# Kernel optimization log

Hardware: AMD Instinct MI355X
Metric: run time of the kernel (lower is better)

The kernel has to match this reference:

```python
import jax, jax.numpy as jnp
import numpy as np

MAX_ITER = 3


def setup_inputs() -> dict:
    key = jax.random.key(0)
    B, S = 8, 128
    k1, k2, k3, k4 = jax.random.split(key, 4)
    return {
        's_edge': jax.random.normal(k1, (B, S, S), jnp.float32),
        's_sib': jax.random.normal(k2, (B, S, S, S), jnp.float32),
        's_cop': jax.random.normal(k3, (B, S, S, S), jnp.float32),
        's_grd': jax.random.normal(k4, (B, S, S, S), jnp.float32),
        'mask': jnp.ones((B, S, S), dtype=bool),
    }


def _msg_update(q, m_old, s):
    # q: [2,S,S,B]; m_old, s: [2|_,S,S,S,B]
    m = q[:, :, :, None, :] - m_old                      # [2,S,S,S,B]
    low = jnp.logaddexp(m[0], m[1])                      # label-0 message
    high = jnp.logaddexp(m[0], m[1] + s)                 # label-1 message (adds 2nd-order score)
    z = jnp.logaddexp(low, high)                         # log_softmax over the 2-way label axis
    return jnp.stack([low - z, high - z])


def _lbp(s_edge, s_sib, s_cop, s_grd, mask, max_iter):
    B, S, _ = mask.shape
    hs = jnp.broadcast_to(jnp.arange(S)[:, None], (S, S))   # row index i
    ms = jnp.broadcast_to(jnp.arange(S)[None, :], (S, S))   # col index j
    maskT = jnp.transpose(mask, (2, 1, 0))                   # [S,S,B] (j,i,B)
    mask2o = maskT[:, None] & maskT[:, :, None]              # [S,S,S,B]
    ar = jnp.arange(S)
    mask2o = mask2o & (hs[..., None] != ar)[..., None]
    mask2o = mask2o & (ms[..., None] != ar)[..., None]
    mask2o = mask2o.astype(s_edge.dtype)                     # [S,S,S,B]

    # s_edge -> [2, j, i, B]; second-order scores -> [j, i, k, B]
    se = jnp.stack([jnp.zeros_like(s_edge), s_edge])
    se = jnp.transpose(se, (0, 3, 2, 1))
    sib = jnp.transpose(s_sib, (2, 1, 3, 0))
    cop = jnp.transpose(s_cop, (2, 1, 3, 0))
    grd = jnp.transpose(s_grd, (2, 1, 3, 0))

    q = se
    zero = jnp.zeros((2, S, S, S, B), dtype=s_edge.dtype)
    m_sib, m_cop, m_grd = zero, zero, zero
    for _ in range(max_iter):
        q = jax.nn.log_softmax(q, axis=0)
        m_sib = _msg_update(q, m_sib, sib)
        m_cop = _msg_update(q, m_cop, cop)
        m_grd = _msg_update(q, m_grd, grd)
        agg = jnp.swapaxes(m_sib + m_cop + m_grd, 2, 3) * mask2o
        q = se + agg.sum(3)                                  # [2,S,S,B]
    return jnp.transpose(q, (3, 2, 1, 0))                     # [B,S,S,2]


def reference(s_edge, s_sib, s_cop, s_grd, mask):
    logits = _lbp(s_edge, s_sib, s_cop, s_grd, mask, MAX_ITER)
    return jax.nn.softmax(logits, axis=-1)[..., 1]            # marginals [B,S,S]
```

## Files before the change

kernel.cpp:

```cpp
#include <hip/hip_runtime.h>


#define TS 128
#define SS (TS * TS)
#define NREG 3

typedef float    f2v __attribute__((ext_vector_type(2)));
typedef _Float16 h2v __attribute__((ext_vector_type(2)));

constexpr float LOG2E = 1.4426950408889634f;

__device__ __forceinline__ float rcpf(float x)   { return __builtin_amdgcn_rcpf(x); }
__device__ __forceinline__ float clampe(float e) { return fminf(fmaxf(e, -126.0f), 60.0f); }
__device__ __forceinline__ float rfl(float x) {
    return __int_as_float(__builtin_amdgcn_readfirstlane(__float_as_int(x)));
}

__global__ void mask_probe(const unsigned char* __restrict__ m, int n, int* __restrict__ f) {
    __shared__ int s1, s23;
    if (threadIdx.x == 0) { s1 = 0; s23 = 0; }
    __syncthreads();
    unsigned a1 = 0, a23 = 0;
    const int n16 = n >> 4;
    const uint4* m4 = (const uint4*)m;
    for (int i = threadIdx.x; i < n16; i += 1024) {
        const uint4 v = m4[i];
        const unsigned o = v.x | v.y | v.z | v.w;
        a1  |= o & 0x0000FF00u;
        a23 |= o & 0xFFFF0000u;
    }
    for (int i = (n16 << 4) + threadIdx.x; i < n; i += 1024) {
        const unsigned char b = m[i];
        const int r = i & 3;
        if (r == 1) a1 |= b;
        if (r >= 2) a23 |= b;
    }
    if (__any(a1 != 0)  && (threadIdx.x & 63) == 0) atomicOr(&s1, 1);
    if (__any(a23 != 0) && (threadIdx.x & 63) == 0) atomicOr(&s23, 1);
    __syncthreads();
    if (threadIdx.x == 0) { f[0] = s1; f[1] = s23; }
}

__global__ __launch_bounds__(1024, 8)
__attribute__((amdgpu_waves_per_eu(8, 8)))
void lbp_fused(const float* __restrict__ s_edge,
               const float* __restrict__ sib,
               const float* __restrict__ cop,
               const float* __restrict__ grd,
               const void* __restrict__ mask,
               const int* __restrict__ flags,
               float* __restrict__ outp)
{
    __shared__ _Float16 FLs[8 - NREG][16][TS];
    __shared__ _Float16 FLc[8 - NREG][16][TS];
    __shared__ _Float16 FLg[8 - NREG][16][TS];
    __shared__ float red[16][TS];
    __shared__ float q0s[TS], p1s[TS], r1s[TS], g1s[TS], g2s[TS];
    __shared__ unsigned char mrow[TS];

    const int bj = blockIdx.x;
    const int b  = bj >> 7;
    const int j  = bj & (TS - 1);
    const int t  = threadIdx.x;
    const int lane = t & 63;
    const int wv = t >> 6;
    const int ka = 2 * lane, kb = 2 * lane + 1;

    if (t < TS) {
        const int i = t;
        const int idx = (b * TS + i) * TS + j;
        const float q0 = LOG2E * s_edge[idx];
        q0s[i] = q0;
        const int f1 = flags[0], f23 = flags[1];
        unsigned char mv;
        if (f1)       mv = ((const unsigned char*)mask)[idx] != 0;
        else if (f23) mv = ((const float*)mask)[idx] != 0.0f;
        else          mv = ((const int*)mask)[idx]   != 0;
        mrow[i] = mv;
        const float p1 = exp2f(clampe(-q0));
        p1s[i] = p1;
        r1s[i] = rcpf(1.0f + p1);
    }
    __syncthreads();

    const size_t gbase = (size_t)b * (TS * SS) + (size_t)j * TS + (size_t)wv * SS + ka;

    h2v Fs[NREG], Fc[NREG], Fg[NREG];
    float a0 = 0.0f, a1 = 0.0f;
    f2v vs = *(const f2v*)(sib + gbase);
    f2v vc = *(const f2v*)(cop + gbase);
    f2v vg = *(const f2v*)(grd + gbase);
    #pragma unroll
    for (int r = 0; r < 8; ++r) {
        f2v nvs, nvc, nvg;
        if (r < 7) {
            const size_t g = gbase + (size_t)(16 * (r + 1)) * SS;
            nvs = *(const f2v*)(sib + g);
            nvc = *(const f2v*)(cop + g);
            nvg = *(const f2v*)(grd + g);
        }
        const int i = 16 * r + wv;
        f2v fs, fc, fg;
        fs[0] = exp2f(LOG2E * vs[0]);  fs[1] = exp2f(LOG2E * vs[1]);
        fc[0] = exp2f(LOG2E * vc[0]);  fc[1] = exp2f(LOG2E * vc[1]);
        fg[0] = exp2f(LOG2E * vg[0]);  fg[1] = exp2f(LOG2E * vg[1]);
        if (r < NREG) {
            Fs[r] = __builtin_convertvector(fs, h2v);
            Fc[r] = __builtin_convertvector(fc, h2v);
            Fg[r] = __builtin_convertvector(fg, h2v);
        } else {
            *(h2v*)&FLs[r - NREG][wv][ka] = __builtin_convertvector(fs, h2v);
            *(h2v*)&FLc[r - NREG][wv][ka] = __builtin_convertvector(fc, h2v);
            *(h2v*)&FLg[r - NREG][wv][ka] = __builtin_convertvector(fg, h2v);
        }
        if ((mrow[i] != 0) && (i != j)) {
            const float p1 = rfl(p1s[i]), r1 = rfl(r1s[i]);
            const float l0 = __log2f(((p1 + fs[0]) * r1) * ((p1 + fc[0]) * r1)
                                     * ((p1 + fg[0]) * r1));
            const float l1 = __log2f(((p1 + fs[1]) * r1) * ((p1 + fc[1]) * r1)
                                     * ((p1 + fg[1]) * r1));
            if (i != ka) a0 += l0;
            if (i != kb) a1 += l1;
        }
        vs = nvs; vc = nvc; vg = nvg;
    }

    { f2v v; v[0] = a0; v[1] = a1; *(f2v*)&red[wv][ka] = v; }
    __syncthreads();
    if (t < TS) {
        float tot = 0.0f;
        #pragma unroll
        for (int w = 0; w < 16; ++w) tot += red[w][t];
        const float q1 = q0s[t] + (mrow[t] ? tot : 0.0f);
        g1s[t] = exp2f(clampe(-q1));
    }
    __syncthreads();

    a0 = 0.0f; a1 = 0.0f;
    #pragma unroll
    for (int r = 0; r < 8; ++r) {
        const int i = 16 * r + wv;
        if ((mrow[i] != 0) && (i != j)) {
            const float p1 = rfl(p1s[i]), r1 = rfl(r1s[i]), g1 = rfl(g1s[i]);
            f2v fs, fc, fg;
            if (r < NREG) {
                fs = __builtin_convertvector(Fs[r], f2v);
                fc = __builtin_convertvector(Fc[r], f2v);
                fg = __builtin_convertvector(Fg[r], f2v);
            } else {
                fs = __builtin_convertvector(*(const h2v*)&FLs[r - NREG][wv][ka], f2v);
                fc = __builtin_convertvector(*(const h2v*)&FLc[r - NREG][wv][ka], f2v);
                fg = __builtin_convertvector(*(const h2v*)&FLg[r - NREG][wv][ka], f2v);
            }
            float l[2];
            #pragma unroll
            for (int c = 0; c < 2; ++c) {
                float p, us, uc, ug;
                us = (p1 + fs[c]) * r1;  p = us * g1;  us = (p + fs[c]) * rcpf(1.0f + p);
                uc = (p1 + fc[c]) * r1;  p = uc * g1;  uc = (p + fc[c]) * rcpf(1.0f + p);
                ug = (p1 + fg[c]) * r1;  p = ug * g1;  ug = (p + fg[c]) * rcpf(1.0f + p);
                l[c] = __log2f(us * uc * ug);
            }
            if (i != ka) a0 += l[0];
            if (i != kb) a1 += l[1];
        }
    }

    { f2v v; v[0] = a0; v[1] = a1; *(f2v*)&red[wv][ka] = v; }
    __syncthreads();
    if (t < TS) {
        float tot = 0.0f;
        #pragma unroll
        for (int w = 0; w < 16; ++w) tot += red[w][t];
        const float q2 = q0s[t] + (mrow[t] ? tot : 0.0f);
        g2s[t] = exp2f(clampe(-q2));
    }
    __syncthreads();

    a0 = 0.0f; a1 = 0.0f;
    #pragma unroll
    for (int r = 0; r < 8; ++r) {
        const int i = 16 * r + wv;
        if ((mrow[i] != 0) && (i != j)) {
            const float p1 = rfl(p1s[i]), r1 = rfl(r1s[i]);
            const float g1 = rfl(g1s[i]), g2 = rfl(g2s[i]);
            f2v fs, fc, fg;
            if (r < NREG) {
                fs = __builtin_convertvector(Fs[r], f2v);
                fc = __builtin_convertvector(Fc[r], f2v);
                fg = __builtin_convertvector(Fg[r], f2v);
            } else {
                fs = __builtin_convertvector(*(const h2v*)&FLs[r - NREG][wv][ka], f2v);
                fc = __builtin_convertvector(*(const h2v*)&FLc[r - NREG][wv][ka], f2v);
                fg = __builtin_convertvector(*(const h2v*)&FLg[r - NREG][wv][ka], f2v);
            }
            float l[2];
            #pragma unroll
            for (int c = 0; c < 2; ++c) {
                float p, us, uc, ug;
                us = (p1 + fs[c]) * r1;  p = us * g1;  us = (p + fs[c]) * rcpf(1.0f + p);
                p = us * g2;  us = (p + fs[c]) * rcpf(1.0f + p);
                uc = (p1 + fc[c]) * r1;  p = uc * g1;  uc = (p + fc[c]) * rcpf(1.0f + p);
                p = uc * g2;  uc = (p + fc[c]) * rcpf(1.0f + p);
                ug = (p1 + fg[c]) * r1;  p = ug * g1;  ug = (p + fg[c]) * rcpf(1.0f + p);
                p = ug * g2;  ug = (p + fg[c]) * rcpf(1.0f + p);
                l[c] = __log2f(us * uc * ug);
            }
            if (i != ka) a0 += l[0];
            if (i != kb) a1 += l[1];
        }
    }

    { f2v v; v[0] = a0; v[1] = a1; *(f2v*)&red[wv][ka] = v; }
    __syncthreads();
    if (t < TS) {
        float tot = 0.0f;
        #pragma unroll
        for (int w = 0; w < 16; ++w) tot += red[w][t];
        const float q3 = q0s[t] + (mrow[t] ? tot : 0.0f);
        outp[(b * TS + t) * TS + j] = 1.0f / (1.0f + exp2f(clampe(-q3)));
    }
}

extern "C" void kernel_launch(void* const* d_in, const int* in_sizes, int n_in,
                              void* d_out, int out_size, void* d_ws, size_t ws_size,
                              hipStream_t stream) {
    const float* s_edge = (const float*)d_in[0];
    const float* sib    = (const float*)d_in[1];
    const float* cop    = (const float*)d_in[2];
    const float* grd    = (const float*)d_in[3];
    const void*  mask   = d_in[4];
    float* out = (float*)d_out;

    const int Bn = in_sizes[0] / (TS * TS);
    const int nMask = in_sizes[4];

    int* flags = (int*)d_ws;

    mask_probe<<<1, 1024, 0, stream>>>((const unsigned char*)mask, nMask, flags);
    lbp_fused<<<Bn * TS, 1024, 0, stream>>>(s_edge, sib, cop, grd, mask, flags, out);
}
```

Measured before the change: 70.94 us.

## Fold masking into unit factors and algebraically simplify message recurrences

Masked or diagonal entries now get exponent factor 1.0, which yields a zero log contribution, so the per-row branches in all three iterations are gone and the loops become branch-free. The first-iteration normalisation is hoisted into a precomputed per-row 3*log2(1+p1) term. The second and third iterations fold the first-step update into FMA forms with per-row constants, replacing several reciprocals with a pair of logs or one reciprocal. The exponent clamp upper bound is lowered to 30, trading some extra log work for fewer divides and less divergence, with some numeric risk from the reformulated products.

```diff
diff --git a/kernel.cpp b/kernel.cpp
--- a/kernel.cpp
+++ b/kernel.cpp
@@ -11,7 +11,7 @@
 constexpr float LOG2E = 1.4426950408889634f;
 
 __device__ __forceinline__ float rcpf(float x)   { return __builtin_amdgcn_rcpf(x); }
-__device__ __forceinline__ float clampe(float e) { return fminf(fmaxf(e, -126.0f), 60.0f); }
+__device__ __forceinline__ float clampe(float e) { return fminf(fmaxf(e, -126.0f), 30.0f); }
 __device__ __forceinline__ float rfl(float x) {
     return __int_as_float(__builtin_amdgcn_readfirstlane(__float_as_int(x)));
 }
@@ -55,7 +55,7 @@
     __shared__ _Float16 FLc[8 - NREG][16][TS];
     __shared__ _Float16 FLg[8 - NREG][16][TS];
     __shared__ float red[16][TS];
-    __shared__ float q0s[TS], p1s[TS], r1s[TS], g1s[TS], g2s[TS];
+    __shared__ float q0s[TS], p1s[TS], r1s[TS], lp3s[TS], g1s[TS], g2s[TS];
     __shared__ unsigned char mrow[TS];
 
     const int bj = blockIdx.x;
@@ -78,8 +78,9 @@
         else          mv = ((const int*)mask)[idx]   != 0;
         mrow[i] = mv;
         const float p1 = exp2f(clampe(-q0));
-        p1s[i] = p1;
-        r1s[i] = rcpf(1.0f + p1);
+        p1s[i]  = p1;
+        r1s[i]  = rcpf(1.0f + p1);
+        lp3s[i] = 3.0f * __log2f(1.0f + p1);
     }
     __syncthreads();
 
@@ -100,10 +101,15 @@
             nvg = *(const f2v*)(grd + g);
         }
         const int i = 16 * r + wv;
+        const bool live = (mrow[i] != 0) && (i != j);
         f2v fs, fc, fg;
-        fs[0] = exp2f(LOG2E * vs[0]);  fs[1] = exp2f(LOG2E * vs[1]);
-        fc[0] = exp2f(LOG2E * vc[0]);  fc[1] = exp2f(LOG2E * vc[1]);
-        fg[0] = exp2f(LOG2E * vg[0]);  fg[1] = exp2f(LOG2E * vg[1]);
+        #pragma unroll
+        for (int c = 0; c < 2; ++c) {
+            const bool on = live && (i != ka + c);
+            fs[c] = on ? exp2f(LOG2E * vs[c]) : 1.0f;
+            fc[c] = on ? exp2f(LOG2E * vc[c]) : 1.0f;
+            fg[c] = on ? exp2f(LOG2E * vg[c]) : 1.0f;
+        }
         if (r < NREG) {
             Fs[r] = __builtin_convertvector(fs, h2v);
             Fc[r] = __builtin_convertvector(fc, h2v);
@@ -113,15 +119,9 @@
             *(h2v*)&FLc[r - NREG][wv][ka] = __builtin_convertvector(fc, h2v);
             *(h2v*)&FLg[r - NREG][wv][ka] = __builtin_convertvector(fg, h2v);
         }
-        if ((mrow[i] != 0) && (i != j)) {
-            const float p1 = rfl(p1s[i]), r1 = rfl(r1s[i]);
-            const float l0 = __log2f(((p1 + fs[0]) * r1) * ((p1 + fc[0]) * r1)
-                                     * ((p1 + fg[0]) * r1));
-            const float l1 = __log2f(((p1 + fs[1]) * r1) * ((p1 + fc[1]) * r1)
-                                     * ((p1 + fg[1]) * r1));
-            if (i != ka) a0 += l0;
-            if (i != kb) a1 += l1;
-        }
+        const float p1 = rfl(p1s[i]), lp3 = rfl(lp3s[i]);
+        a0 += __log2f((p1 + fs[0]) * (p1 + fc[0]) * (p1 + fg[0])) - lp3;
+        a1 += __log2f((p1 + fs[1]) * (p1 + fc[1]) * (p1 + fg[1])) - lp3;
         vs = nvs; vc = nvc; vg = nvg;
     }
 
@@ -140,30 +140,30 @@
     #pragma unroll
     for (int r = 0; r < 8; ++r) {
         const int i = 16 * r + wv;
-        if ((mrow[i] != 0) && (i != j)) {
-            const float p1 = rfl(p1s[i]), r1 = rfl(r1s[i]), g1 = rfl(g1s[i]);
-            f2v fs, fc, fg;
-            if (r < NREG) {
-                fs = __builtin_convertvector(Fs[r], f2v);
-                fc = __builtin_convertvector(Fc[r], f2v);
-                fg = __builtin_convertvector(Fg[r], f2v);
-            } else {
-                fs = __builtin_convertvector(*(const h2v*)&FLs[r - NREG][wv][ka], f2v);
-                fc = __builtin_convertvector(*(const h2v*)&FLc[r - NREG][wv][ka], f2v);
-                fg = __builtin_convertvector(*(const h2v*)&FLg[r - NREG][wv][ka], f2v);
-            }
-            float l[2];
-            #pragma unroll
-            for (int c = 0; c < 2; ++c) {
-                float p, us, uc, ug;
-                us = (p1 + fs[c]) * r1;  p = us * g1;  us = (p + fs[c]) * rcpf(1.0f + p);
-                uc = (p1 + fc[c]) * r1;  p = uc * g1;  uc = (p + fc[c]) * rcpf(1.0f + p);
-                ug = (p1 + fg[c]) * r1;  p = ug * g1;  ug = (p + fg[c]) * rcpf(1.0f + p);
-                l[c] = __log2f(us * uc * ug);
-            }
-            if (i != ka) a0 += l[0];
-            if (i != kb) a1 += l[1];
-        }
+        const float m1  = rfl(r1s[i]) * rfl(g1s[i]);
+        const float c1  = rfl(p1s[i]) * m1;
+        const float m1p = 1.0f + m1;
+        const float c1p = 1.0f + c1;
+        f2v fs, fc, fg;
+        if (r < NREG) {
+            fs = __builtin_convertvector(Fs[r], f2v);
+            fc = __builtin_convertvector(Fc[r], f2v);
+            fg = __builtin_convertvector(Fg[r], f2v);
+        } else {
+            fs = __builtin_convertvector(*(const h2v*)&FLs[r - NREG][wv][ka], f2v);
+            fc = __builtin_convertvector(*(const h2v*)&FLc[r - NREG][wv][ka], f2v);
+            fg = __builtin_convertvector(*(const h2v*)&FLg[r - NREG][wv][ka], f2v);
+        }
+        float l[2];
+        #pragma unroll
+        for (int c = 0; c < 2; ++c) {
+            const float as = fmaf(fs[c], m1p, c1), bs = fmaf(fs[c], m1, c1p);
+            const float ac = fmaf(fc[c], m1p, c1), bc = fmaf(fc[c], m1, c1p);
+            const float ag = fmaf(fg[c], m1p, c1), bg = fmaf(fg[c], m1, c1p);
+            l[c] = __log2f(as * ac * ag) - __log2f(bs * bc * bg);
+        }
+        a0 += l[0];
+        a1 += l[1];
     }
 
     { f2v v; v[0] = a0; v[1] = a1; *(f2v*)&red[wv][ka] = v; }
@@ -181,34 +181,33 @@
     #pragma unroll
     for (int r = 0; r < 8; ++r) {
         const int i = 16 * r + wv;
-        if ((mrow[i] != 0) && (i != j)) {
-            const float p1 = rfl(p1s[i]), r1 = rfl(r1s[i]);
-            const float g1 = rfl(g1s[i]), g2 = rfl(g2s[i]);
-            f2v fs, fc, fg;
-            if (r < NREG) {
-                fs = __builtin_convertvector(Fs[r], f2v);
-                fc = __builtin_convertvector(Fc[r], f2v);
-                fg = __builtin_convertvector(Fg[r], f2v);
-            } else {
-                fs = __builtin_convertvector(*(const h2v*)&FLs[r - NREG][wv][ka], f2v);
-                fc = __builtin_convertvector(*(const h2v*)&FLc[r - NREG][wv][ka], f2v);
-                fg = __builtin_convertvector(*(const h2v*)&FLg[r - NREG][wv][ka], f2v);
-            }
-            float l[2];
-            #pragma unroll
-            for (int c = 0; c < 2; ++c) {
-                float p, us, uc, ug;
-                us = (p1 + fs[c]) * r1;  p = us * g1;  us = (p + fs[c]) * rcpf(1.0f + p);
-                p = us * g2;  us = (p + fs[c]) * rcpf(1.0f + p);
-                uc = (p1 + fc[c]) * r1;  p = uc * g1;  uc = (p + fc[c]) * rcpf(1.0f + p);
-                p = uc * g2;  uc = (p + fc[c]) * rcpf(1.0f + p);
-                ug = (p1 + fg[c]) * r1;  p = ug * g1;  ug = (p + fg[c]) * rcpf(1.0f + p);
-                p = ug * g2;  ug = (p + fg[c]) * rcpf(1.0f + p);
-                l[c] = __log2f(us * uc * ug);
-            }
-            if (i != ka) a0 += l[0];
-            if (i != kb) a1 += l[1];
-        }
+        const float m1  = rfl(r1s[i]) * rfl(g1s[i]);
+        const float c1  = rfl(p1s[i]) * m1;
+        const float m1p = 1.0f + m1;
+        const float c1p = 1.0f + c1;
+        const float g2  = rfl(g2s[i]);
+        f2v fs, fc, fg;
+        if (r < NREG) {
+            fs = __builtin_convertvector(Fs[r], f2v);
+            fc = __builtin_convertvector(Fc[r], f2v);
+            fg = __builtin_convertvector(Fg[r], f2v);
+        } else {
+            fs = __builtin_convertvector(*(const h2v*)&FLs[r - NREG][wv][ka], f2v);
+            fc = __builtin_convertvector(*(const h2v*)&FLc[r - NREG][wv][ka], f2v);
+            fg = __builtin_convertvector(*(const h2v*)&FLg[r - NREG][wv][ka], f2v);
+        }
+        float l[2];
+        #pragma unroll
+        for (int c = 0; c < 2; ++c) {
+            const float us = fmaf(fs[c], m1p, c1) * rcpf(fmaf(fs[c], m1, c1p));
+            const float uc = fmaf(fc[c], m1p, c1) * rcpf(fmaf(fc[c], m1, c1p));
+            const float ug = fmaf(fg[c], m1p, c1) * rcpf(fmaf(fg[c], m1, c1p));
+            const float ps = us * g2, pc = uc * g2, pg = ug * g2;
+            l[c] = __log2f((ps + fs[c]) * (pc + fc[c]) * (pg + fg[c]))
+                 - __log2f((1.0f + ps) * (1.0f + pc) * (1.0f + pg));
+        }
+        a0 += l[0];
+        a1 += l[1];
     }
 
     { f2v v; v[0] = a0; v[1] = a1; *(f2v*)&red[wv][ka] = v; }
```

Result: faster. 68.32 us (-3.7%).
